# Optimization experiments

Hardware: AMD Instinct MI355X
Metric: run time of the kernel (lower is better)

The kernel has to match this reference:

```python
import jax, jax.numpy as jnp
import numpy as np

B, CDD, HIS, S, L, F, K = 32, 5, 100, 20, 3, 150, 18
NNEWS, RDIM = 10000, 256


def _maxpool3(x):
    # kernel [3,3,3], stride [3,3,3], no padding (torch MaxPool3d default)
    return jax.lax.reduce_window(x, -jnp.inf, jax.lax.max,
                                 (1, 1, 3, 3, 3), (1, 1, 3, 3, 3), 'VALID')


def setup_inputs() -> dict:
    key = jax.random.key(0)
    ks = jax.random.split(key, 10)
    return {
        'cdd_id': jax.random.randint(ks[0], (B, CDD), 0, NNEWS),
        'his_id': jax.random.randint(ks[1], (B, HIS), 0, NNEWS),
        'news_repr_table': jax.random.normal(ks[2], (NNEWS, RDIM), jnp.float32),
        'news_embedding_table': jax.random.normal(ks[3], (NNEWS, S * L * F), jnp.float32),
        'conv1_w': jax.random.normal(ks[4], (32, 3, 3, 3, 3), jnp.float32) * 0.1,
        'conv1_b': jax.random.normal(ks[5], (32,), jnp.float32) * 0.1,
        'conv2_w': jax.random.normal(ks[6], (16, 32, 3, 3, 3), jnp.float32) * 0.1,
        'conv2_b': jax.random.normal(ks[7], (16,), jnp.float32) * 0.1,
        'ltr_w': jax.random.normal(ks[8], (1, 128), jnp.float32) * 0.1,
        'ltr_b': jax.random.normal(ks[9], (1,), jnp.float32) * 0.1,
    }


def reference(cdd_id, his_id, news_repr_table, news_embedding_table,
              conv1_w, conv1_b, conv2_w, conv2_b, ltr_w, ltr_b):
    cdd_repr = news_repr_table[cdd_id]                    # [B,CDD,R]
    his_repr = news_repr_table[his_id]                    # [B,HIS,R]
    cdd_emb = news_embedding_table[cdd_id].reshape(B, CDD, S, L, F)
    his_emb = news_embedding_table[his_id]                # [B,HIS,S*L*F]

    # attention scores; original applies softmax then sorts the (detached)
    # weights -- softmax is monotone per row so argsort on logits is identical
    attn = jnp.einsum('bcr,bhr->bch', cdd_repr, his_repr)  # [B,CDD,HIS]
    topk_idx = jnp.argsort(-attn, axis=-1)[..., :K]        # [B,CDD,K]

    # direct gather (replaces the one_hot @ embedding matmul, same math)
    his_act = his_emb[jnp.arange(B)[:, None, None], topk_idx]  # [B,CDD,K,S*L*F]
    his_act = his_act.reshape(B, CDD, K, S, L, F)

    # fusion tensor at each dilation level
    cdd_t = cdd_emb.transpose(0, 1, 3, 2, 4)       # [B,CDD,L,S,F]
    his_t = his_act.transpose(0, 1, 2, 4, 3, 5)    # [B,CDD,K,L,S,F]
    fusion = jnp.einsum('bclsf,bckltf->bcklst', cdd_t, his_t) / np.sqrt(F).astype(np.float32)
    x = fusion.reshape(B * CDD, K, L, S, S).transpose(0, 2, 1, 3, 4)  # [B*CDD,L,K,S,S]

    dn = ('NCDHW', 'OIDHW', 'NCDHW')
    pad1 = [(1, 1)] * 3
    x = jax.lax.conv_general_dilated(x, conv1_w, (1, 1, 1), pad1, dimension_numbers=dn)
    x = jax.nn.relu(x + conv1_b[None, :, None, None, None])
    x = _maxpool3(x)                                # [B*CDD,32,6,6,6]
    x = jax.lax.conv_general_dilated(x, conv2_w, (1, 1, 1), pad1, dimension_numbers=dn)
    x = jax.nn.relu(x + conv2_b[None, :, None, None, None])
    x = _maxpool3(x)                                # [B*CDD,16,2,2,2]

    feat = x.reshape(B, CDD, -1)                    # [B,CDD,128]
    score = jnp.einsum('bcd,od->bco', feat, ltr_w)[..., 0] + ltr_b[0]  # [B,CDD]
    return jax.nn.log_softmax(score, axis=1)
```

## Files before the change

### kernel.cpp

```cpp
#include <hip/hip_runtime.h>
#include <hip/hip_bf16.h>
#include <math.h>

#define B_    32
#define CDD_  5
#define HIS_  100
#define S_    20
#define L_    3
#define F_    150
#define K_    18
#define RDIM_ 256
#define ROWE_ 9000
#define NBC_  160

typedef __attribute__((ext_vector_type(8))) short short8;
typedef __attribute__((ext_vector_type(4))) float f32x4;
typedef __attribute__((ext_vector_type(2))) float f32x2;

static __device__ __forceinline__ unsigned short f2bf(float x) {
  union { float f; unsigned u; } v; v.f = x;
  unsigned r = v.u + 0x7fffu + ((v.u >> 16) & 1u);
  return (unsigned short)(r >> 16);
}

static __device__ __forceinline__ unsigned pack2bf(float a, float b) {
  return (unsigned)f2bf(a) | ((unsigned)f2bf(b) << 16);
}

__global__ __launch_bounds__(256) void attn_topk_kernel(
    const int* __restrict__ cdd_id, const int* __restrict__ his_id,
    const float* __restrict__ repr, int* __restrict__ gid,
    float* __restrict__ score,
    const float* __restrict__ w1, const float* __restrict__ w2,
    float* __restrict__ w1t, float* __restrict__ w2t) {
  int bc = blockIdx.x;
  int b  = bc / CDD_;
  int tid = threadIdx.x, lane = tid & 63, wave = tid >> 6;

  int gidx = bc * 256 + tid;
  if (gidx < 2592) {
    int oc = gidx / 81, j = gidx % 81;
    w1t[j * 32 + oc] = w1[gidx];
  } else if (gidx < 2592 + 13824) {
    int i2 = gidx - 2592;
    int oc = i2 / 864, r = i2 % 864;
    w2t[r * 16 + oc] = w2[i2];
  }

  __shared__ float cddv[RDIM_];
  __shared__ float sattn[128];
  int cid = cdd_id[bc];
  cddv[tid] = repr[(size_t)cid * RDIM_ + tid];
  if (tid < 28) sattn[100 + tid] = -INFINITY;
  __syncthreads();

  float4 cv = *(const float4*)(cddv + lane * 4);
  for (int h = wave; h < HIS_; h += 4) {
    const float4* row = (const float4*)(repr + (size_t)his_id[b * HIS_ + h] * RDIM_);
    float4 rv = row[lane];
    float p = cv.x * rv.x;
    p = fmaf(cv.y, rv.y, p);
    p = fmaf(cv.z, rv.z, p);
    p = fmaf(cv.w, rv.w, p);
    #pragma unroll
    for (int off = 32; off >= 1; off >>= 1) p += __shfl_xor(p, off);
    if (lane == 0) sattn[h] = p;
  }
  __syncthreads();

  if (wave == 0) {
    float v0 = sattn[lane], v1 = sattn[lane + 64];
    for (int k = 0; k < K_; k++) {
      float bv; int bi;
      if (v1 > v0) { bv = v1; bi = lane + 64; } else { bv = v0; bi = lane; }
      #pragma unroll
      for (int off = 32; off >= 1; off >>= 1) {
        float ov = __shfl_xor(bv, off);
        int   oi = __shfl_xor(bi, off);
        if (ov > bv || (ov == bv && oi < bi)) { bv = ov; bi = oi; }
      }
      if (lane == 0) gid[bc * K_ + k] = his_id[b * HIS_ + bi];
      if (bi == lane)      v0 = -INFINITY;
      if (bi == lane + 64) v1 = -INFINITY;
    }
  }
  if (tid == 0) score[bc] = 0.f;
}

__global__ __launch_bounds__(256) void fusion_kernel(
    const int* __restrict__ cdd_id, const int* __restrict__ gid,
    const float* __restrict__ emb, float* __restrict__ x1) {
  int bck = (blockIdx.x & 7) * 360 + (blockIdx.x >> 3);
  int bc = bck / K_, k = bck % K_;
  __shared__ unsigned short a_sh[3 * 32 * 160];
  __shared__ unsigned short b_sh[3 * 32 * 160];
  int tid = threadIdx.x;

  unsigned* az = (unsigned*)a_sh;
  unsigned* bz = (unsigned*)b_sh;
  for (int i = tid; i < 480; i += 256) {
    int l = i / 160, r = i % 160;
    int srow = r / 5, j = r % 5;
    int idx = (l * 32 + srow) * 80 + 75 + j;
    az[idx] = 0u; bz[idx] = 0u;
  }

  const float* crow = emb + (size_t)cdd_id[bc] * ROWE_;
  const float* hrow = emb + (size_t)gid[bck] * ROWE_;
  for (int p = tid; p < 2250; p += 256) {
    int e0 = p * 4;
    int s0 = e0 / 450, r0 = e0 % 450;
    int l0 = r0 / 150, f0 = r0 % 150;
    int e2 = e0 + 2;
    int s2 = e2 / 450, r2 = e2 % 450;
    int l2 = r2 / 150, f2 = r2 % 150;
    float4 cv = *(const float4*)(crow + e0);
    float4 hv = *(const float4*)(hrow + e0);
    int d0 = (l0 * 32 + s0) * 80 + (f0 >> 1);
    int d2 = (l2 * 32 + s2) * 80 + (f2 >> 1);
    az[d0] = pack2bf(cv.x, cv.y);
    az[d2] = pack2bf(cv.z, cv.w);
    bz[d0] = pack2bf(hv.x, hv.y);
    bz[d2] = pack2bf(hv.z, hv.w);
  }
  __syncthreads();

  int wave = tid >> 6, lane = tid & 63;
  int m15 = lane & 15, quad = lane >> 4;
  const float scale = 0.0816496580927726f;
  for (int j = wave; j < 12; j += 4) {
    int l = j >> 2, mt = (j >> 1) & 1, nt = j & 1;
    f32x4 acc = {0.f, 0.f, 0.f, 0.f};
    int abase = (l * 32 + mt * 16 + m15) * 160 + quad * 8;
    int bbase = (l * 32 + nt * 16 + m15) * 160 + quad * 8;
    #pragma unroll
    for (int kb = 0; kb < 5; kb++) {
      short8 af = *(const short8*)(a_sh + abase + kb * 32);
      short8 bf = *(const short8*)(b_sh + bbase + kb * 32);
      acc = __builtin_amdgcn_mfma_f32_16x16x32_bf16(af, bf, acc, 0, 0, 0);
    }
    int t = nt * 16 + m15;
    if (t < 20) {
      size_t base = ((size_t)(bc * 3 + l) * K_ + k) * 400;
      #pragma unroll
      for (int reg = 0; reg < 4; reg++) {
        int s = mt * 16 + quad * 4 + reg;
        if (s < 20) x1[base + s * 20 + t] = acc[reg] * scale;
      }
    }
  }
}

__global__ __launch_bounds__(256) void conv1_kernel(
    const float* __restrict__ x1, const float* __restrict__ w1t,
    const float* __restrict__ b1, float* __restrict__ p1) {
  int bid = blockIdx.x;
  int n = bid / 6, dp = bid % 6;
  __shared__ float tile[3 * 5 * 22 * 22];
  __shared__ unsigned pooled[32 * 36];
  int tid = threadIdx.x;

  for (int i = tid; i < 7260; i += 256) {
    int c = i / 2420; int r = i % 2420;
    int dd = r / 484; r %= 484;
    int hh = r / 22, ww = r % 22;
    int d = dp * 3 + dd - 1, h = hh - 1, w = ww - 1;
    float v = 0.f;
    if (d >= 0 && d < 18 && h >= 0 && h < 20 && w >= 0 && w < 20)
      v = x1[((size_t)(n * 3 + c) * K_ + d) * 400 + h * 20 + w];
    tile[i] = v;
  }
  for (int i = tid; i < 1152; i += 256) pooled[i] = 0u;
  __syncthreads();

  const f32x2* b1v = (const f32x2*)b1;
  for (int pos = tid; pos < 972; pos += 256) {
    int dl = pos / 324; int r = pos % 324;
    int h = r / 18, w = r % 18;
    f32x2 acc[16];
    #pragma unroll
    for (int i = 0; i < 16; i++) acc[i] = b1v[i];

    for (int c = 0; c < 3; c++) {
      const float* tc = tile + (c * 5 + dl) * 484 + h * 22 + w;
      const float* wc = w1t + c * 27 * 32;
      #pragma unroll
      for (int kd = 0; kd < 3; kd++)
        #pragma unroll
        for (int kh = 0; kh < 3; kh++)
          #pragma unroll
          for (int kw = 0; kw < 3; kw++) {
            float iv = tc[kd * 484 + kh * 22 + kw];
            f32x2 ivv = {iv, iv};
            const f32x2* wp = (const f32x2*)(wc + (kd * 9 + kh * 3 + kw) * 32);
            #pragma unroll
            for (int i = 0; i < 16; i++)
              acc[i] = __builtin_elementwise_fma(ivv, wp[i], acc[i]);
          }
    }
    int pbase = (h / 3) * 6 + (w / 3);
    #pragma unroll
    for (int i = 0; i < 16; i++) {
      atomicMax(&pooled[(2 * i) * 36 + pbase],     __float_as_uint(fmaxf(acc[i].x, 0.f)));
      atomicMax(&pooled[(2 * i + 1) * 36 + pbase], __float_as_uint(fmaxf(acc[i].y, 0.f)));
    }
  }
  __syncthreads();
  for (int i = tid; i < 1152; i += 256) {
    int oc = i / 36; int r = i % 36;
    p1[(size_t)(n * 32 + oc) * 216 + dp * 36 + r] = __uint_as_float(pooled[i]);
  }
}

__global__ __launch_bounds__(256) void conv2_kernel(
    const float* __restrict__ p1, const float* __restrict__ w2t,
    const float* __restrict__ b2, const float* __restrict__ lw,
    float* __restrict__ score) {
  int bid = blockIdx.x;
  int n = bid / 2, og = bid % 2;
  __shared__ float tile[32 * 8 * 8 * 8];
  __shared__ unsigned pooled[64];
  int tid = threadIdx.x;

  for (int i = tid; i < 32 * 512; i += 256) tile[i] = 0.f;
  if (tid < 64) pooled[tid] = 0u;
  __syncthreads();
  for (int i = tid; i < 32 * 216; i += 256) {
    int c = i / 216; int r = i % 216;
    int d = r / 36; r %= 36;
    int h = r / 6, w = r % 6;
    tile[c * 512 + (d + 1) * 64 + (h + 1) * 8 + (w + 1)] =
        p1[(size_t)n * 32 * 216 + i];
  }
  __syncthreads();

  if (tid < 216) {
    int d = tid / 36; int r = tid % 36;
    int h = r / 6, w = r % 6;
    f32x2 acc[4];
    #pragma unroll
    for (int i = 0; i < 4; i++)
      acc[i] = (f32x2){b2[og * 8 + 2 * i], b2[og * 8 + 2 * i + 1]};
    for (int c = 0; c < 32; c++) {
      const float* tc = tile + c * 512 + d * 64 + h * 8 + w;
      const float* wc = w2t + c * 27 * 16 + og * 8;
      #pragma unroll
      for (int kd = 0; kd < 3; kd++)
        #pragma unroll
        for (int kh = 0; kh < 3; kh++)
          #pragma unroll
          for (int kw = 0; kw < 3; kw++) {
            float iv = tc[kd * 64 + kh * 8 + kw];
            f32x2 ivv = {iv, iv};
            const f32x2* wp = (const f32x2*)(wc + (kd * 9 + kh * 3 + kw) * 16);
            #pragma unroll
            for (int i = 0; i < 4; i++)
              acc[i] = __builtin_elementwise_fma(ivv, wp[i], acc[i]);
          }
    }
    int pb = (d / 3) * 4 + (h / 3) * 2 + (w / 3);
    #pragma unroll
    for (int i = 0; i < 4; i++) {
      atomicMax(&pooled[(2 * i) * 8 + pb],     __float_as_uint(fmaxf(acc[i].x, 0.f)));
      atomicMax(&pooled[(2 * i + 1) * 8 + pb], __float_as_uint(fmaxf(acc[i].y, 0.f)));
    }
  }
  __syncthreads();

  if (tid < 64) {
    int oc = tid / 8, pb = tid % 8;
    float contrib = __uint_as_float(pooled[tid]) * lw[(og * 8 + oc) * 8 + pb];
    #pragma unroll
    for (int off = 32; off >= 1; off >>= 1) contrib += __shfl_xor(contrib, off);
    if (tid == 0) atomicAdd(&score[n], contrib);
  }
}

__global__ __launch_bounds__(64) void softmax_kernel(
    const float* __restrict__ score, const float* __restrict__ lb,
    float* __restrict__ out) {
  int b = threadIdx.x;
  if (b < B_) {
    float s[CDD_];
    float mx = -INFINITY;
    #pragma unroll
    for (int c = 0; c < CDD_; c++) {
      s[c] = score[b * CDD_ + c] + lb[0];
      mx = fmaxf(mx, s[c]);
    }
    float sum = 0.f;
    #pragma unroll
    for (int c = 0; c < CDD_; c++) sum += expf(s[c] - mx);
    float lse = mx + logf(sum);
    #pragma unroll
    for (int c = 0; c < CDD_; c++) out[b * CDD_ + c] = s[c] - lse;
  }
}

extern "C" void kernel_launch(void* const* d_in, const int* in_sizes, int n_in,
                              void* d_out, int out_size, void* d_ws, size_t ws_size,
                              hipStream_t stream) {
  const int*   cdd_id = (const int*)d_in[0];
  const int*   his_id = (const int*)d_in[1];
  const float* repr   = (const float*)d_in[2];
  const float* emb    = (const float*)d_in[3];
  const float* w1     = (const float*)d_in[4];
  const float* b1     = (const float*)d_in[5];
  const float* w2     = (const float*)d_in[6];
  const float* b2     = (const float*)d_in[7];
  const float* lw     = (const float*)d_in[8];
  const float* lb     = (const float*)d_in[9];
  float* out = (float*)d_out;

  char* ws = (char*)d_ws;
  int*   gid   = (int*)ws;
  float* score = (float*)(ws + 11520);
  float* x1    = (float*)(ws + 12160);
  float* p1    = (float*)(ws + 12160 + 13824000);
  float* w1t   = (float*)(ws + 12160 + 13824000 + 4423680);
  float* w2t   = (float*)(ws + 12160 + 13824000 + 4423680 + 10368);

  attn_topk_kernel<<<NBC_, 256, 0, stream>>>(cdd_id, his_id, repr, gid, score,
                                             w1, w2, w1t, w2t);
  fusion_kernel<<<NBC_ * K_, 256, 0, stream>>>(cdd_id, gid, emb, x1);
  conv1_kernel<<<NBC_ * 6, 256, 0, stream>>>(x1, w1t, b1, p1);
  conv2_kernel<<<NBC_ * 2, 256, 0, stream>>>(p1, w2t, b2, lw, score);
  softmax_kernel<<<1, 64, 0, stream>>>(score, lb, out);
}
```

Measured before the change: 607.8 us.

## Register-tile conv1 over pooling window width and fuse softmax into conv2

Conv1 threads now each compute three adjacent outputs along w, reusing loaded input rows and weights across them and reducing the w-dimension of the max-pool in registers before LDS atomics; block size becomes 320. The separate softmax kernel is removed and replaced by a per-batch completion counter in conv2, where the last finishing block computes log-softmax. This reduces LDS loads, atomics, and one launch, at the cost of higher register pressure and a threadfence/atomic counter protocol.

After: 673.8 us. 1.11x slower.

```diff
diff --git a/kernel.cpp b/kernel.cpp
--- a/kernel.cpp
+++ b/kernel.cpp
@@ -30,7 +30,7 @@
 __global__ __launch_bounds__(256) void attn_topk_kernel(
     const int* __restrict__ cdd_id, const int* __restrict__ his_id,
     const float* __restrict__ repr, int* __restrict__ gid,
-    float* __restrict__ score,
+    float* __restrict__ score, int* __restrict__ scnt,
     const float* __restrict__ w1, const float* __restrict__ w2,
     float* __restrict__ w1t, float* __restrict__ w2t) {
   int bc = blockIdx.x;
@@ -84,7 +84,10 @@
       if (bi == lane + 64) v1 = -INFINITY;
     }
   }
-  if (tid == 0) score[bc] = 0.f;
+  if (tid == 0) {
+    score[bc] = 0.f;
+    if (bc < B_) scnt[bc] = 0;
+  }
 }
 
 __global__ __launch_bounds__(256) void fusion_kernel(
@@ -151,7 +154,7 @@
   }
 }
 
-__global__ __launch_bounds__(256) void conv1_kernel(
+__global__ __launch_bounds__(320) void conv1_kernel(
     const float* __restrict__ x1, const float* __restrict__ w1t,
     const float* __restrict__ b1, float* __restrict__ p1) {
   int bid = blockIdx.x;
@@ -160,7 +163,7 @@
   __shared__ unsigned pooled[32 * 36];
   int tid = threadIdx.x;
 
-  for (int i = tid; i < 7260; i += 256) {
+  for (int i = tid; i < 7260; i += 320) {
     int c = i / 2420; int r = i % 2420;
     int dd = r / 484; r %= 484;
     int hh = r / 22, ww = r % 22;
@@ -170,43 +173,57 @@
       v = x1[((size_t)(n * 3 + c) * K_ + d) * 400 + h * 20 + w];
     tile[i] = v;
   }
-  for (int i = tid; i < 1152; i += 256) pooled[i] = 0u;
+  for (int i = tid; i < 1152; i += 320) pooled[i] = 0u;
   __syncthreads();
 
   const f32x2* b1v = (const f32x2*)b1;
-  for (int pos = tid; pos < 972; pos += 256) {
-    int dl = pos / 324; int r = pos % 324;
-    int h = r / 18, w = r % 18;
-    f32x2 acc[16];
-    #pragma unroll
-    for (int i = 0; i < 16; i++) acc[i] = b1v[i];
+  for (int job = tid; job < 324; job += 320) {
+    int dl = job / 108; int r = job % 108;
+    int h = r / 6, pw = r % 6;
+    int w0 = pw * 3;
+    f32x2 acc[3][16];
+    #pragma unroll
+    for (int j = 0; j < 3; j++)
+      #pragma unroll
+      for (int i = 0; i < 16; i++) acc[j][i] = b1v[i];
 
     for (int c = 0; c < 3; c++) {
-      const float* tc = tile + (c * 5 + dl) * 484 + h * 22 + w;
+      const float* tc = tile + (c * 5 + dl) * 484 + h * 22 + w0;
       const float* wc = w1t + c * 27 * 32;
       #pragma unroll
       for (int kd = 0; kd < 3; kd++)
         #pragma unroll
-        for (int kh = 0; kh < 3; kh++)
+        for (int kh = 0; kh < 3; kh++) {
+          const float* tr = tc + kd * 484 + kh * 22;
+          float rv[5];
+          #pragma unroll
+          for (int q = 0; q < 5; q++) rv[q] = tr[q];
           #pragma unroll
           for (int kw = 0; kw < 3; kw++) {
-            float iv = tc[kd * 484 + kh * 22 + kw];
-            f32x2 ivv = {iv, iv};
             const f32x2* wp = (const f32x2*)(wc + (kd * 9 + kh * 3 + kw) * 32);
             #pragma unroll
-            for (int i = 0; i < 16; i++)
-              acc[i] = __builtin_elementwise_fma(ivv, wp[i], acc[i]);
+            for (int i = 0; i < 16; i++) {
+              f32x2 wv = wp[i];
+              #pragma unroll
+              for (int j = 0; j < 3; j++) {
+                f32x2 iv2 = {rv[j + kw], rv[j + kw]};
+                acc[j][i] = __builtin_elementwise_fma(iv2, wv, acc[j][i]);
+              }
+            }
           }
-    }
-    int pbase = (h / 3) * 6 + (w / 3);
+        }
+    }
+    int pbase = (h / 3) * 6 + pw;
     #pragma unroll
     for (int i = 0; i < 16; i++) {
-      atomicMax(&pooled[(2 * i) * 36 + pbase],     __float_as_uint(fmaxf(acc[i].x, 0.f)));
-      atomicMax(&pooled[(2 * i + 1) * 36 + pbase], __float_as_uint(fmaxf(acc[i].y, 0.f)));
-    }
-  }
-  __syncthreads();
-  for (int i = tid; i < 1152; i += 256) {
+      float mx = fmaxf(acc[0][i].x, fmaxf(acc[1][i].x, acc[2][i].x));
+      float my = fmaxf(acc[0][i].y, fmaxf(acc[1][i].y, acc[2][i].y));
+      atomicMax(&pooled[(2 * i) * 36 + pbase],     __float_as_uint(fmaxf(mx, 0.f)));
+      atomicMax(&pooled[(2 * i + 1) * 36 + pbase], __float_as_uint(fmaxf(my, 0.f)));
+    }
+  }
+  __syncthreads();
+  for (int i = tid; i < 1152; i += 320) {
     int oc = i / 36; int r = i % 36;
     p1[(size_t)(n * 32 + oc) * 216 + dp * 36 + r] = __uint_as_float(pooled[i]);
   }
@@ -215,7 +232,8 @@
 __global__ __launch_bounds__(256) void conv2_kernel(
     const float* __restrict__ p1, const float* __restrict__ w2t,
     const float* __restrict__ b2, const float* __restrict__ lw,
-    float* __restrict__ score) {
+    const float* __restrict__ lb, float* __restrict__ score,
+    int* __restrict__ scnt, float* __restrict__ out) {
   int bid = blockIdx.x;
   int n = bid / 2, og = bid % 2;
   __shared__ float tile[32 * 8 * 8 * 8];
@@ -274,26 +292,27 @@
     for (int off = 32; off >= 1; off >>= 1) contrib += __shfl_xor(contrib, off);
     if (tid == 0) atomicAdd(&score[n], contrib);
   }
-}
-
-__global__ __launch_bounds__(64) void softmax_kernel(
-    const float* __restrict__ score, const float* __restrict__ lb,
-    float* __restrict__ out) {
-  int b = threadIdx.x;
-  if (b < B_) {
-    float s[CDD_];
-    float mx = -INFINITY;
-    #pragma unroll
-    for (int c = 0; c < CDD_; c++) {
-      s[c] = score[b * CDD_ + c] + lb[0];
-      mx = fmaxf(mx, s[c]);
-    }
-    float sum = 0.f;
-    #pragma unroll
-    for (int c = 0; c < CDD_; c++) sum += expf(s[c] - mx);
-    float lse = mx + logf(sum);
-    #pragma unroll
-    for (int c = 0; c < CDD_; c++) out[b * CDD_ + c] = s[c] - lse;
+
+  if (tid == 0) {
+    __threadfence();
+    int b = n / CDD_;
+    int old = atomicAdd(&scnt[b], 1);
+    if (old == 2 * CDD_ - 1) {
+      __threadfence();
+      float s[CDD_];
+      float mx = -INFINITY;
+      #pragma unroll
+      for (int c = 0; c < CDD_; c++) {
+        s[c] = score[b * CDD_ + c] + lb[0];
+        mx = fmaxf(mx, s[c]);
+      }
+      float sum = 0.f;
+      #pragma unroll
+      for (int c = 0; c < CDD_; c++) sum += expf(s[c] - mx);
+      float lse = mx + logf(sum);
+      #pragma unroll
+      for (int c = 0; c < CDD_; c++) out[b * CDD_ + c] = s[c] - lse;
+    }
   }
 }
 
@@ -319,11 +338,11 @@
   float* p1    = (float*)(ws + 12160 + 13824000);
   float* w1t   = (float*)(ws + 12160 + 13824000 + 4423680);
   float* w2t   = (float*)(ws + 12160 + 13824000 + 4423680 + 10368);
+  int*   scnt  = (int*)(ws + 12160 + 13824000 + 4423680 + 10368 + 55296);
 
   attn_topk_kernel<<<NBC_, 256, 0, stream>>>(cdd_id, his_id, repr, gid, score,
-                                             w1, w2, w1t, w2t);
+                                             scnt, w1, w2, w1t, w2t);
   fusion_kernel<<<NBC_ * K_, 256, 0, stream>>>(cdd_id, gid, emb, x1);
-  conv1_kernel<<<NBC_ * 6, 256, 0, stream>>>(x1, w1t, b1, p1);
-  conv2_kernel<<<NBC_ * 2, 256, 0, stream>>>(p1, w2t, b2, lw, score);
-  softmax_kernel<<<1, 64, 0, stream>>>(score, lb, out);
-}
+  conv1_kernel<<<NBC_ * 6, 320, 0, stream>>>(x1, w1t, b1, p1);
+  conv2_kernel<<<NBC_ * 2, 256, 0, stream>>>(p1, w2t, b2, lw, lb, score, scnt, out);
+}
```
